# Kernel optimization log

Hardware: AMD Instinct MI355X
Metric: run time of the kernel (lower is better)

## Reference

```python
import jax, jax.numpy as jnp
import numpy as np

N_BRANCH, N_LAYER = 4, 3
B, T, D_IN = 4, 1024, 32
D_MODEL, D_INNER, D_STATE, D_CONV, DT_RANK = 128, 256, 16, 4, 8
EMBED = 64
MAX_NORM = 10.0  # safe_expmap0 tangent-norm clip
EPS = 1e-7


def setup_inputs() -> dict:
    key = jax.random.key(0)
    ks = jax.random.split(key, 12)
    def nrm(k, shp, s=0.02):
        return s * jax.random.normal(k, shp, dtype=jnp.float32)
    A_init = jnp.log(jnp.arange(1, D_STATE + 1, dtype=jnp.float32))
    return {
        "trend": jax.random.normal(ks[0], (B, T, D_IN), jnp.float32),
        "seasonal_coarse": jax.random.normal(ks[1], (B, T, D_IN), jnp.float32),
        "seasonal_fine": jax.random.normal(ks[2], (B, T, D_IN), jnp.float32),
        "residual": jax.random.normal(ks[3], (B, T, D_IN), jnp.float32),
        "W_ip": nrm(ks[4], (N_BRANCH, D_IN, D_MODEL)),
        "b_ip": jnp.zeros((N_BRANCH, D_MODEL), jnp.float32),
        "W_in": nrm(ks[5], (N_BRANCH, N_LAYER, D_MODEL, 2 * D_INNER)),
        "conv_w": nrm(ks[6], (N_BRANCH, N_LAYER, D_INNER, D_CONV), 0.1),
        "conv_b": jnp.zeros((N_BRANCH, N_LAYER, D_INNER), jnp.float32),
        "W_x": nrm(ks[7], (N_BRANCH, N_LAYER, D_INNER, DT_RANK + 2 * D_STATE)),
        "W_dt": nrm(ks[8], (N_BRANCH, N_LAYER, DT_RANK, D_INNER), 0.1),
        "b_dt": jnp.full((N_BRANCH, N_LAYER, D_INNER), -4.6, jnp.float32),  # softplus ~ 0.01
        "A_log": jnp.broadcast_to(A_init, (N_BRANCH, N_LAYER, D_INNER, D_STATE)),
        "D_param": jnp.ones((N_BRANCH, N_LAYER, D_INNER), jnp.float32),
        "W_out": nrm(ks[9], (N_BRANCH, N_LAYER, D_INNER, D_MODEL)),
        "W_op": nrm(ks[10], (N_BRANCH, D_MODEL, EMBED)),
        "b_op": jnp.zeros((N_BRANCH, EMBED), jnp.float32),
        "eff_scale": jnp.asarray(0.1, jnp.float32),
    }


def _mamba_layer(x, Win, cw, cb, Wx, Wdt, bdt, Alog, Dp, Wout):
    # x: [B, T, d_model]
    Tlen = x.shape[1]
    xz = x @ Win                                   # [B,T,2*di]
    xp, z = jnp.split(xz, 2, axis=-1)
    # causal depthwise conv1d, kernel D_CONV
    xpad = jnp.pad(xp, ((0, 0), (D_CONV - 1, 0), (0, 0)))
    xc = sum(xpad[:, k:k + Tlen, :] * cw[:, k] for k in range(D_CONV))
    xc = jax.nn.silu(xc + cb)                      # [B,T,di]
    dbl = xc @ Wx                                  # [B,T,r+2s]
    dt = jax.nn.softplus(dbl[..., :DT_RANK] @ Wdt + bdt)   # [B,T,di]
    Bm = dbl[..., DT_RANK:DT_RANK + D_STATE]       # [B,T,s]
    Cm = dbl[..., DT_RANK + D_STATE:]              # [B,T,s]
    A = -jnp.exp(Alog)                             # [di,s]
    dA = jnp.exp(dt[..., None] * A)                # [B,T,di,s]
    dBx = (dt * xc)[..., None] * Bm[:, :, None, :] # [B,T,di,s]

    def step(h, inp):
        dA_t, dBx_t, C_t = inp
        h = dA_t * h + dBx_t
        return h, jnp.einsum('bds,bs->bd', h, C_t)

    h0 = jnp.zeros((x.shape[0], D_INNER, D_STATE), x.dtype)
    _, ys = jax.lax.scan(step, h0, (jnp.swapaxes(dA, 0, 1),
                                     jnp.swapaxes(dBx, 0, 1),
                                     jnp.swapaxes(Cm, 0, 1)))
    y = jnp.swapaxes(ys, 0, 1) + Dp * xc
    return (y * jax.nn.silu(z)) @ Wout


def _embed(x, Wip, bip, Wins, cws, cbs, Wxs, Wdts, bdts, Alogs, Dps, Wouts, Wop, bop):
    h = x @ Wip + bip
    for l in range(N_LAYER):
        h = _mamba_layer(h, Wins[l], cws[l], cbs[l], Wxs[l], Wdts[l], bdts[l],
                         Alogs[l], Dps[l], Wouts[l])
    return h.mean(axis=1) @ Wop + bop              # [B, EMBED]


def _expmap0(v):
    # safe expmap0 on Lorentz (k=1): clip tangent norm at MAX_NORM
    n = jnp.linalg.norm(v, axis=-1, keepdims=True)
    nc = jnp.clip(n, EPS, MAX_NORM)
    v = v * (nc / jnp.maximum(n, EPS))
    return jnp.concatenate([jnp.cosh(nc), jnp.sinh(nc) / nc * v], axis=-1)


def _projx(x):
    sp = x[..., 1:]
    t = jnp.sqrt(1.0 + jnp.sum(sp * sp, axis=-1, keepdims=True))
    return jnp.concatenate([t, sp], axis=-1)


def _logmap0(x):
    sp = x[..., 1:]
    t = jnp.maximum(x[..., :1], 1.0 + EPS)
    d = jnp.arccosh(t)
    spn = jnp.maximum(jnp.linalg.norm(sp, axis=-1, keepdims=True), EPS)
    return d * sp / spn


def _forward(trend, seasonal_coarse, seasonal_fine, residual,
             W_ip, b_ip, W_in, conv_w, conv_b, W_x, W_dt, b_dt,
             A_log, D_param, W_out, W_op, b_op, eff_scale):
    xs = [trend, seasonal_coarse, seasonal_fine, residual]
    z_t = [
        _embed(xs[b], W_ip[b], b_ip[b], W_in[b], conv_w[b], conv_b[b], W_x[b],
               W_dt[b], b_dt[b], A_log[b], D_param[b], W_out[b], W_op[b], b_op[b])
        for b in range(N_BRANCH)
    ]
    es = jnp.tanh(eff_scale)
    z_h = [_projx(_expmap0(z * es)) for z in z_t]
    us = [_logmap0(zh) for zh in z_h]
    combined_tangent = us[0] + us[1] + us[2] + us[3]
    combined_h = _projx(_expmap0(combined_tangent * es))
    return (*z_t, *z_h, combined_tangent, combined_h)


def reference(trend, seasonal_coarse, seasonal_fine, residual,
              W_ip, b_ip, W_in, conv_w, conv_b, W_x, W_dt, b_dt,
              A_log, D_param, W_out, W_op, b_op, eff_scale):
    return _forward(trend, seasonal_coarse, seasonal_fine, residual,
                    W_ip, b_ip, W_in, conv_w, conv_b, W_x, W_dt, b_dt,
                    A_log, D_param, W_out, W_op, b_op, eff_scale)
```

## Files before the change

kernel.cpp:

```cpp
#include <hip/hip_runtime.h>
#include <math.h>

#define NBR 4
#define NLAY 3
#define Bk 4
#define Tk 1024
#define DIN 32
#define DMODEL 128
#define DINNER 256
#define DSTATE 16
#define DTRANK 8
#define EMBEDk 64
#define BT (Bk*Tk)
#define EPSF 1e-7f
#define MAXNF 10.0f
#define LCH 64
#define NCH (Tk/LCH)
#define UF 8
#define NWB 320

typedef __bf16 bf16x8 __attribute__((ext_vector_type(8)));
typedef float  f32x4  __attribute__((ext_vector_type(4)));
typedef unsigned short u16x8 __attribute__((ext_vector_type(8)));

__device__ __forceinline__ float siluf(float x){ return x / (1.f + __expf(-x)); }
__device__ __forceinline__ float softplusf(float x){ return (x > 20.f) ? x : log1pf(__expf(x)); }
__device__ __forceinline__ unsigned short f2b(float x){
    union { float f; unsigned u; } v; v.f = x;
    unsigned r = v.u + 0x7FFF + ((v.u >> 16) & 1);
    return (unsigned short)(r >> 16);
}
__device__ __forceinline__ float b2f(unsigned short u){
    union { unsigned u; float f; } v; v.u = ((unsigned)u) << 16; return v.f;
}

__device__ __forceinline__ void gll16(const void* g, void* l){
    __builtin_amdgcn_global_load_lds(
        (const __attribute__((address_space(1))) unsigned int*)g,
        (__attribute__((address_space(3))) unsigned int*)l,
        16, 0, 0);
}

__device__ __forceinline__ void dA_pow(float q, float* dA){
    dA[0] = q;             dA[1] = q * q;
    dA[2] = dA[1] * dA[0]; dA[3] = dA[1] * dA[1];
    dA[4] = dA[3] * dA[0]; dA[5] = dA[3] * dA[1];
    dA[6] = dA[3] * dA[2]; dA[7] = dA[3] * dA[3];
    #pragma unroll
    for (int s = 8; s < 16; ++s) dA[s] = dA[s - 8] * dA[7];
}
__device__ __forceinline__ void dA_exp(float dtv, const float* Aa, float* dA){
    #pragma unroll
    for (int s = 0; s < 16; ++s) dA[s] = __expf(dtv * Aa[s]);
}

template<int MODE>
__global__ __launch_bounds__(256) void bgemm_k(
    const unsigned short* __restrict__ Ab, long aBr, int K,
    const unsigned short* __restrict__ Bt, long bBr,
    float* __restrict__ C0, long c0Br,
    float* __restrict__ C1, long c1Br,
    unsigned short* __restrict__ Cb, long cbBr,
    const float* __restrict__ bias, long biasBr)
{
    const int br = blockIdx.z;
    Ab += (long)br * aBr;
    Bt += (long)br * bBr;
    if (MODE == 3) C0 += (long)br * c0Br;
    if (MODE == 0 || MODE == 3) C1 += (long)br * c1Br;
    if (MODE == 0) Cb += (long)br * cbBr;
    if (MODE == 3) bias += (long)br * biasBr;
    const int m0 = blockIdx.x * 64, n0 = blockIdx.y * 64;
    __shared__ __align__(16) unsigned short As[8 * 64 * 8];
    __shared__ __align__(16) unsigned short Bs[8 * 64 * 8];
    const int tid = threadIdx.x;
    const int lane = tid & 63, w = tid >> 6;
    const int wm = w >> 1, wn = w & 1;
    const int quad = lane >> 4, l15 = lane & 15;
    f32x4 acc00 = {0,0,0,0}, acc01 = {0,0,0,0}, acc10 = {0,0,0,0}, acc11 = {0,0,0,0};
    for (int kc = 0; kc < K; kc += 64) {
        #pragma unroll
        for (int it = 0; it < 2; ++it) {
            const int kch = w + it * 4;
            gll16(Ab + (long)(m0 + lane) * K + kc + kch * 8, &As[(kch * 64) * 8]);
            gll16(Bt + (long)(n0 + lane) * K + kc + kch * 8, &Bs[(kch * 64) * 8]);
        }
        __syncthreads();
        #pragma unroll
        for (int k0 = 0; k0 < 64; k0 += 32) {
            const int kch = (k0 >> 3) + quad;
            bf16x8 a0 = *(const bf16x8*)&As[(kch * 64 + wm * 32 +      l15) * 8];
            bf16x8 a1 = *(const bf16x8*)&As[(kch * 64 + wm * 32 + 16 + l15) * 8];
            bf16x8 b0 = *(const bf16x8*)&Bs[(kch * 64 + wn * 32 +      l15) * 8];
            bf16x8 b1 = *(const bf16x8*)&Bs[(kch * 64 + wn * 32 + 16 + l15) * 8];
            acc00 = __builtin_amdgcn_mfma_f32_16x16x32_bf16(a0, b0, acc00, 0, 0, 0);
            acc01 = __builtin_amdgcn_mfma_f32_16x16x32_bf16(a0, b1, acc01, 0, 0, 0);
            acc10 = __builtin_amdgcn_mfma_f32_16x16x32_bf16(a1, b0, acc10, 0, 0, 0);
            acc11 = __builtin_amdgcn_mfma_f32_16x16x32_bf16(a1, b1, acc11, 0, 0, 0);
        }
        __syncthreads();
    }
    #pragma unroll
    for (int e = 0; e < 4; ++e) {
        f32x4 a = (e == 0) ? acc00 : (e == 1) ? acc01 : (e == 2) ? acc10 : acc11;
        const int msub = (e >> 1) * 16, nsub = (e & 1) * 16;
        const int col = n0 + wn * 32 + nsub + l15;
        #pragma unroll
        for (int r = 0; r < 4; ++r) {
            const int row = m0 + wm * 32 + msub + quad * 4 + r;
            const float v = a[r];
            if (MODE == 0) {
                if (n0 < 256) Cb[(long)row * 256 + col] = f2b(v);
                else          C1[(long)row * 256 + (col - 256)] = siluf(v);
            } else {
                if (col < 256)      C0[(long)row * 256 + col] = softplusf(v + bias[col]);
                else if (col < 288) C1[(long)row * 32 + (col - 256)] = v;
            }
        }
    }
}

__global__ __launch_bounds__(256) void prepT_k(
    const float* __restrict__ W, unsigned short* __restrict__ o,
    int Kd, int Nd, long wBr, long oBr)
{
    const int br = blockIdx.z;
    W += (long)br * wBr; o += (long)br * oBr;
    const int n0 = blockIdx.x * 64, k0 = blockIdx.y * 64;
    __shared__ float tile[64][65];
    const int t = threadIdx.x;
    #pragma unroll
    for (int i = 0; i < 16; ++i) {
        int idx = t + i * 256;
        int kl = idx >> 6, nl = idx & 63;
        tile[kl][nl] = W[(long)(k0 + kl) * Nd + n0 + nl];
    }
    __syncthreads();
    #pragma unroll
    for (int i = 0; i < 16; ++i) {
        int idx = t + i * 256;
        int nl = idx >> 6, kl = idx & 63;
        o[(long)(n0 + nl) * Kd + k0 + kl] = f2b(tile[kl][nl]);
    }
}

__global__ __launch_bounds__(256) void sgemmW_k(
    const float* __restrict__ Wout, const float* __restrict__ Win,
    float* __restrict__ Wtmp)
{
    const int z = blockIdx.z, p = z >> 2, br = z & 3;
    const float* A  = Wout + (long)(br * NLAY + p) * DINNER * DMODEL;
    const float* Bw = Win  + (long)(br * NLAY + p + 1) * DMODEL * 512;
    float* C = Wtmp + (long)z * DINNER * 512;
    const int m0 = blockIdx.x * 64, n0 = blockIdx.y * 64;
    __shared__ float As[32][68];
    __shared__ float Bs[32][68];
    const int tid = threadIdx.x;
    const int tx = tid & 15, ty = tid >> 4;
    float acc[4][4] = {};
    for (int kc = 0; kc < DMODEL; kc += 32) {
        #pragma unroll
        for (int it = 0; it < 2; ++it) {
            int id = tid + it * 256;
            int r = id >> 3, c4 = (id & 7) << 2;
            float4 v = *(const float4*)(A + (long)(m0 + r) * DMODEL + kc + c4);
            As[c4+0][r] = v.x; As[c4+1][r] = v.y; As[c4+2][r] = v.z; As[c4+3][r] = v.w;
            int rb = id >> 4, cb = (id & 15) << 2;
            *(float4*)&Bs[rb][cb] = *(const float4*)(Bw + (long)(kc + rb) * 512 + n0 + cb);
        }
        __syncthreads();
        #pragma unroll
        for (int kk = 0; kk < 32; ++kk) {
            float4 a4 = *(const float4*)&As[kk][ty << 2];
            float4 b4 = *(const float4*)&Bs[kk][tx << 2];
            float av[4] = {a4.x, a4.y, a4.z, a4.w};
            float bv[4] = {b4.x, b4.y, b4.z, b4.w};
            #pragma unroll
            for (int i = 0; i < 4; ++i)
                #pragma unroll
                for (int j = 0; j < 4; ++j)
                    acc[i][j] = fmaf(av[i], bv[j], acc[i][j]);
        }
        __syncthreads();
    }
    #pragma unroll
    for (int i = 0; i < 4; ++i) {
        int row = m0 + (ty << 2) + i, col = n0 + (tx << 2);
        float4 v4; v4.x = acc[i][0]; v4.y = acc[i][1]; v4.z = acc[i][2]; v4.w = acc[i][3];
        *(float4*)(C + (long)row * 512 + col) = v4;
    }
}

__global__ __launch_bounds__(256) void prepC_k(
    const float* __restrict__ Wx, const float* __restrict__ Wdt,
    unsigned short* __restrict__ o)
{
    const int n = blockIdx.x, bl = blockIdx.y;
    const int k = threadIdx.x;
    const float* WxP = Wx + (long)bl * DINNER * 40;
    float v;
    if (n < 256) {
        const float* WdtP = Wdt + (long)bl * DTRANK * DINNER;
        float s = 0.f;
        #pragma unroll
        for (int r = 0; r < 8; ++r) s = fmaf(WxP[k * 40 + r], WdtP[r * DINNER + n], s);
        v = s;
    } else if (n < 288) {
        v = WxP[k * 40 + 8 + (n - 256)];
    } else {
        v = 0.f;
    }
    o[(long)bl * NWB * DINNER + (long)n * DINNER + k] = f2b(v);
}

__global__ __launch_bounds__(256) void proj_k(
    const float* __restrict__ A0, const float* __restrict__ A1,
    const float* __restrict__ A2, const float* __restrict__ A3,
    const float* __restrict__ Bw, const float* __restrict__ bias,
    unsigned short* __restrict__ Cb)
{
    const int br = blockIdx.z;
    const float* A = (br == 1) ? A1 : (br == 2) ? A2 : (br == 3) ? A3 : A0;
    Bw   += (long)br * DIN * DMODEL;
    bias += (long)br * DMODEL;
    Cb   += (long)br * BT * DMODEL;
    const int m0 = blockIdx.x * 64, n0 = blockIdx.y * 64;
    __shared__ float As[32][68];
    __shared__ float Bs[32][68];
    const int tid = threadIdx.x;
    const int tx = tid & 15, ty = tid >> 4;
    float acc[4][4] = {};
    {
        #pragma unroll
        for (int it = 0; it < 2; ++it) {
            int id = tid + it * 256;
            int r = id >> 3, c4 = (id & 7) << 2;
            float4 v = *(const float4*)(A + (long)(m0 + r) * DIN + c4);
            As[c4+0][r] = v.x; As[c4+1][r] = v.y; As[c4+2][r] = v.z; As[c4+3][r] = v.w;
            int rb = id >> 4, cb = (id & 15) << 2;
            *(float4*)&Bs[rb][cb] = *(const float4*)(Bw + (long)rb * DMODEL + n0 + cb);
        }
        __syncthreads();
        #pragma unroll
        for (int kk = 0; kk < 32; ++kk) {
            float4 a4 = *(const float4*)&As[kk][ty << 2];
            float4 b4 = *(const float4*)&Bs[kk][tx << 2];
            float av[4] = {a4.x, a4.y, a4.z, a4.w};
            float bv[4] = {b4.x, b4.y, b4.z, b4.w};
            #pragma unroll
            for (int i = 0; i < 4; ++i)
                #pragma unroll
                for (int j = 0; j < 4; ++j)
                    acc[i][j] = fmaf(av[i], bv[j], acc[i][j]);
        }
    }
    const int col = n0 + (tx << 2);
    float bs[4];
    #pragma unroll
    for (int j = 0; j < 4; ++j) bs[j] = bias[col + j];
    #pragma unroll
    for (int i = 0; i < 4; ++i) {
        const int row = m0 + (ty << 2) + i;
        #pragma unroll
        for (int j = 0; j < 4; ++j)
            Cb[(long)row * DMODEL + col + j] = f2b(acc[i][j] + bs[j]);
    }
}

__global__ __launch_bounds__(256) void conv_k(
    const unsigned short* __restrict__ xp, const float* __restrict__ cw,
    const float* __restrict__ cb, unsigned short* __restrict__ xcb, int layer)
{
    const int br = blockIdx.y;
    const long base = (long)br * BT * DINNER;
    const long idx8 = ((long)blockIdx.x * 256 + threadIdx.x) * 8;
    const int d0 = (int)(idx8 & (DINNER - 1));
    const long row = idx8 >> 8;
    const int t = (int)(row & (Tk - 1));
    const float* cwp = cw + ((long)(br * NLAY + layer) * DINNER + d0) * 4;
    const float* cbp = cb + (long)(br * NLAY + layer) * DINNER + d0;
    u16x8 in[4];
    #pragma unroll
    for (int k = 0; k < 4; ++k) {
        const int tt = t + k - 3;
        if (tt >= 0) {
            in[k] = *(const u16x8*)(xp + base + idx8 + (long)(k - 3) * DINNER);
        } else {
            #pragma unroll
            for (int j = 0; j < 8; ++j) in[k][j] = 0;
        }
    }
    u16x8 o;
    #pragma unroll
    for (int j = 0; j < 8; ++j) {
        float acc = cbp[j];
        #pragma unroll
        for (int k = 0; k < 4; ++k)
            acc = fmaf(b2f(in[k][j]), cwp[j * 4 + k], acc);
        o[j] = f2b(siluf(acc));
    }
    *(u16x8*)(xcb + base + idx8) = o;
}

__global__ __launch_bounds__(256) void scan1_k(
    const float* __restrict__ dtb, const unsigned short* __restrict__ xcb,
    const float* __restrict__ bcb, const float* __restrict__ Alog,
    float* __restrict__ recbuf, int layer)
{
    const int c = blockIdx.x, b = blockIdx.y, br = blockIdx.z;
    const int d = threadIdx.x;
    const float* Ap = Alog + ((long)(br * NLAY + layer) * DINNER + d) * DSTATE;
    float Aa[16];
    bool pw = true;
    #pragma unroll
    for (int s = 0; s < 16; ++s) {
        Aa[s] = -__expf(Ap[s]);
        pw = pw && (fabsf(Aa[s] + (float)(s + 1)) < 1e-3f);
    }
    const long rbase = (long)br * BT + (long)b * Tk + (long)c * LCH;
    const float* dtp = dtb + rbase * DINNER + d;
    const unsigned short* xcp = xcb + rbase * DINNER + d;
    __shared__ float bcs[LCH * 32];
    {
        const float4* g = (const float4*)(bcb + rbase * 32);
        float4* l = (float4*)bcs;
        l[d] = g[d]; l[d + 256] = g[d + 256];
    }
    float dtc[UF], xcc[UF];
    #pragma unroll
    for (int u = 0; u < UF; ++u) {
        dtc[u] = dtp[(long)u * DINNER];
        xcc[u] = b2f(xcp[(long)u * DINNER]);
    }
    __syncthreads();
    float h[16];
    #pragma unroll
    for (int s = 0; s < 16; ++s) h[s] = 0.f;
    float sumdt = 0.f;
    for (int base = 0; base < LCH; base += UF) {
        const int nb = (base + UF < LCH) ? base + UF : base;
        float dtn[UF], xcn[UF];
        #pragma unroll
        for (int u = 0; u < UF; ++u) {
            dtn[u] = dtp[(long)(nb + u) * DINNER];
            xcn[u] = b2f(xcp[(long)(nb + u) * DINNER]);
        }
        #pragma unroll
        for (int u = 0; u < UF; ++u) {
            const int t = base + u;
            const float dtv = dtc[u];
            const float dtxc = dtv * xcc[u];
            sumdt += dtv;
            float dA[16];
            if (pw) dA_pow(__expf(-dtv), dA);
            else    dA_exp(dtv, Aa, dA);
            const float* bcT = bcs + t * 32;
            #pragma unroll
            for (int s = 0; s < 16; ++s)
                h[s] = fmaf(dA[s], h[s], dtxc * bcT[s]);
        }
        #pragma unroll
        for (int u = 0; u < UF; ++u) { dtc[u] = dtn[u]; xcc[u] = xcn[u]; }
    }
    float* sb = recbuf + (((long)(br * 4 + b) * (NCH - 1) + c) * 17) * 256 + d;
    #pragma unroll
    for (int s = 0; s < 16; ++s) sb[s * 256] = h[s];
    sb[16 * 256] = sumdt;
}

__global__ __launch_bounds__(256) void scan3_k(
    const float* __restrict__ dtb, const unsigned short* __restrict__ xcb,
    const float* __restrict__ bcb, const float* __restrict__ zb,
    const float* __restrict__ Alog, const float* __restrict__ Dpar,
    const float* __restrict__ recbuf, unsigned short* __restrict__ yzb, int layer)
{
    const int c = blockIdx.x, b = blockIdx.y, br = blockIdx.z;
    const int d = threadIdx.x;
    const float* Ap = Alog + ((long)(br * NLAY + layer) * DINNER + d) * DSTATE;
    float Aa[16];
    bool pw = true;
    #pragma unroll
    for (int s = 0; s < 16; ++s) {
        Aa[s] = -__expf(Ap[s]);
        pw = pw && (fabsf(Aa[s] + (float)(s + 1)) < 1e-3f);
    }
    float h[16];
    #pragma unroll
    for (int s = 0; s < 16; ++s) h[s] = 0.f;
    if (c > 0) {
        const float* recB = recbuf + ((long)(br * 4 + b) * (NCH - 1)) * 17 * 256 + d;
        float rh[16], rs;
        #pragma unroll
        for (int s = 0; s < 16; ++s) rh[s] = recB[s * 256];
        rs = recB[16 * 256];
        for (int cc = 0; cc < c; ++cc) {
            float nh[16], ns = 0.f;
            if (cc + 1 < c) {
                const float* r2 = recB + (long)(cc + 1) * 17 * 256;
                #pragma unroll
                for (int s = 0; s < 16; ++s) nh[s] = r2[s * 256];
                ns = r2[16 * 256];
            } else {
                #pragma unroll
                for (int s = 0; s < 16; ++s) nh[s] = 0.f;
            }
            float P[16];
            if (pw) dA_pow(__expf(-rs), P);
            else    dA_exp(rs, Aa, P);
            #pragma unroll
            for (int s = 0; s < 16; ++s) h[s] = fmaf(h[s], P[s], rh[s]);
            #pragma unroll
            for (int s = 0; s < 16; ++s) rh[s] = nh[s];
            rs = ns;
        }
    }
    const float Dp = Dpar[(br * NLAY + layer) * DINNER + d];
    const long rbase = (long)br * BT + (long)b * Tk + (long)c * LCH;
    const float* dtp = dtb + rbase * DINNER + d;
    const unsigned short* xcp = xcb + rbase * DINNER + d;
    const float* zp  = zb  + rbase * DINNER + d;
    unsigned short* yp = yzb + rbase * DINNER + d;
    __shared__ float bcs[LCH * 32];
    {
        const float4* g = (const float4*)(bcb + rbase * 32);
        float4* l = (float4*)bcs;
        l[d] = g[d]; l[d + 256] = g[d + 256];
    }
    float dtc[UF], xcc[UF], zc[UF];
    #pragma unroll
    for (int u = 0; u < UF; ++u) {
        dtc[u] = dtp[(long)u * DINNER];
        xcc[u] = b2f(xcp[(long)u * DINNER]);
        zc[u]  = zp[(long)u * DINNER];
    }
    __syncthreads();
    for (int base = 0; base < LCH; base += UF) {
        const int nb = (base + UF < LCH) ? base + UF : base;
        float dtn[UF], xcn[UF], zn[UF];
        #pragma unroll
        for (int u = 0; u < UF; ++u) {
            dtn[u] = dtp[(long)(nb + u) * DINNER];
            xcn[u] = b2f(xcp[(long)(nb + u) * DINNER]);
            zn[u]  = zp[(long)(nb + u) * DINNER];
        }
        #pragma unroll
        for (int u = 0; u < UF; ++u) {
            const int t = base + u;
            const float dtv = dtc[u], xcv = xcc[u];
            const float dtxc = dtv * xcv;
            float dA[16];
            if (pw) dA_pow(__expf(-dtv), dA);
            else    dA_exp(dtv, Aa, dA);
            const float* bcT = bcs + t * 32;
            #pragma unroll
            for (int s = 0; s < 16; ++s)
                h[s] = fmaf(dA[s], h[s], dtxc * bcT[s]);
            float y0 = 0.f, y1 = 0.f, y2 = 0.f, y3 = 0.f;
            #pragma unroll
            for (int s = 0; s < 16; s += 4) {
                y0 = fmaf(h[s+0], bcT[16+s+0], y0);
                y1 = fmaf(h[s+1], bcT[16+s+1], y1);
                y2 = fmaf(h[s+2], bcT[16+s+2], y2);
                y3 = fmaf(h[s+3], bcT[16+s+3], y3);
            }
            const float y = (y0 + y1) + (y2 + y3) + Dp * xcv;
            yp[(long)t * DINNER] = f2b(y * zc[u]);
        }
        #pragma unroll
        for (int u = 0; u < UF; ++u) { dtc[u] = dtn[u]; xcc[u] = xcn[u]; zc[u] = zn[u]; }
    }
}

__global__ __launch_bounds__(256) void csum1_k(
    const unsigned short* __restrict__ yz, float* __restrict__ part)
{
    const int ch = blockIdx.x, brb = blockIdx.y;
    const int br = brb >> 2, b = brb & 3;
    const long rbase = (long)br * BT + (long)b * Tk + (long)ch * 128;
    const int tid = threadIdx.x;
    const int cg = tid & 31;
    const int ro = tid >> 5;
    const unsigned short* p = yz + (rbase + ro) * DINNER + cg * 8;
    float acc[8] = {0,0,0,0,0,0,0,0};
    for (int it = 0; it < 16; ++it) {
        u16x8 v = *(const u16x8*)(p + (long)it * 8 * DINNER);
        #pragma unroll
        for (int j = 0; j < 8; ++j) acc[j] += b2f(v[j]);
    }
    __shared__ float sm[8][256];
    #pragma unroll
    for (int j = 0; j < 8; ++j) sm[ro][cg * 8 + j] = acc[j];
    __syncthreads();
    float s = 0.f;
    #pragma unroll
    for (int r = 0; r < 8; ++r) s += sm[r][tid];
    part[((long)brb * 8 + ch) * 256 + tid] = s;
}

__global__ __launch_bounds__(256) void csum2_k(
    const float* __restrict__ part, const float* __restrict__ Wout,
    const float* __restrict__ Wop, const float* __restrict__ bop,
    float* __restrict__ outzt)
{
    const int brb = blockIdx.x;
    const int br = brb >> 2, b = brb & 3;
    const int tid = threadIdx.x;
    __shared__ float v[256];
    __shared__ float u[128];
    float s = 0.f;
    #pragma unroll
    for (int ch = 0; ch < 8; ++ch) s += part[((long)brb * 8 + ch) * 256 + tid];
    v[tid] = s * (1.0f / Tk);
    __syncthreads();
    if (tid < 128) {
        const float* W2 = Wout + (long)(br * NLAY + 2) * DINNER * DMODEL;
        float a = 0.f;
        for (int k = 0; k < 256; ++k) a = fmaf(v[k], W2[k * DMODEL + tid], a);
        u[tid] = a;
    }
    __syncthreads();
    if (tid < EMBEDk) {
        float a = bop[br * EMBEDk + tid];
        for (int k = 0; k < 128; ++k)
            a = fmaf(u[k], Wop[(long)br * DMODEL * EMBEDk + k * EMBEDk + tid], a);
        outzt[br * (Bk * EMBEDk) + b * EMBEDk + tid] = a;
    }
}

__global__ __launch_bounds__(64) void final_k(
    const float* __restrict__ zt, float* __restrict__ out, const float* __restrict__ eff)
{
    const float es = tanhf(eff[0]);
    __shared__ float us[NBR][Bk][EMBEDk];
    const int t = threadIdx.x;
    if (t < 16) {
        const int br = t >> 2, b = t & 3;
        const float* z = zt + br * (Bk * EMBEDk) + b * EMBEDk;
        float n2 = 0.f;
        for (int e = 0; e < EMBEDk; ++e) { float v = z[e] * es; n2 = fmaf(v, v, n2); }
        const float n  = sqrtf(n2);
        const float nc = fminf(fmaxf(n, EPSF), MAXNF);
        const float sc = nc / fmaxf(n, EPSF);
        const float sh = sinhf(nc) / nc;
        const float fac = es * sc * sh;
        float* zh = out + 1024 + br * (Bk * (EMBEDk + 1)) + b * (EMBEDk + 1);
        float sp2 = 0.f;
        for (int e = 0; e < EMBEDk; ++e) {
            float spv = z[e] * fac;
            sp2 = fmaf(spv, spv, sp2);
            zh[1 + e] = spv;
            us[br][b][e] = spv;
        }
        const float t0 = sqrtf(1.f + sp2);
        zh[0] = t0;
        const float dd  = acoshf(fmaxf(t0, 1.f + EPSF));
        const float spn = fmaxf(sqrtf(sp2), EPSF);
        const float rr  = dd / spn;
        for (int e = 0; e < EMBEDk; ++e) us[br][b][e] *= rr;
    }
    __syncthreads();
    if (t < 4) {
        const int b = t;
        float ct[EMBEDk];
        float* cto = out + 2064 + b * EMBEDk;
        for (int e = 0; e < EMBEDk; ++e) {
            float v = us[0][b][e] + us[1][b][e] + us[2][b][e] + us[3][b][e];
            ct[e] = v; cto[e] = v;
        }
        float n2 = 0.f;
        for (int e = 0; e < EMBEDk; ++e) { float v = ct[e] * es; n2 = fmaf(v, v, n2); }
        const float n  = sqrtf(n2);
        const float nc = fminf(fmaxf(n, EPSF), MAXNF);
        const float sc = nc / fmaxf(n, EPSF);
        const float sh = sinhf(nc) / nc;
        const float fac = es * sc * sh;
        float* ch = out + 2320 + b * (EMBEDk + 1);
        float sp2 = 0.f;
        for (int e = 0; e < EMBEDk; ++e) {
            float spv = ct[e] * fac;
            sp2 = fmaf(spv, spv, sp2);
            ch[1 + e] = spv;
        }
        ch[0] = sqrtf(1.f + sp2);
    }
}

extern "C" void kernel_launch(void* const* d_in, const int* in_sizes, int n_in,
                              void* d_out, int out_size, void* d_ws, size_t ws_size,
                              hipStream_t stream)
{
    const float* X0 = (const float*)d_in[0];
    const float* X1 = (const float*)d_in[1];
    const float* X2 = (const float*)d_in[2];
    const float* X3 = (const float*)d_in[3];
    const float* W_ip   = (const float*)d_in[4];
    const float* b_ip   = (const float*)d_in[5];
    const float* W_in   = (const float*)d_in[6];
    const float* conv_w = (const float*)d_in[7];
    const float* conv_b = (const float*)d_in[8];
    const float* W_x    = (const float*)d_in[9];
    const float* W_dt   = (const float*)d_in[10];
    const float* b_dt   = (const float*)d_in[11];
    const float* A_log  = (const float*)d_in[12];
    const float* D_par  = (const float*)d_in[13];
    const float* W_out  = (const float*)d_in[14];
    const float* W_op   = (const float*)d_in[15];
    const float* b_op   = (const float*)d_in[16];
    const float* eff    = (const float*)d_in[17];
    float* out = (float*)d_out;
    float* ws  = (float*)d_ws;

    float* buf_z  = ws;
    float* buf_dt = buf_z  + (long)NBR * BT * DINNER;
    float* buf_bc = buf_dt + (long)NBR * BT * DINNER;
    float* part   = buf_bc + (long)NBR * BT * 32;
    float* recbuf = part   + (long)NBR * BT * DMODEL;
    float* Wtmp   = recbuf + (long)16 * (NCH - 1) * 17 * 256;
    unsigned short* h_bf  = (unsigned short*)(Wtmp + (long)8 * DINNER * 512);
    unsigned short* xp_bf = h_bf  + (long)NBR * BT * DMODEL;
    unsigned short* xc_bf = xp_bf + (long)NBR * BT * DINNER;
    unsigned short* yz_bf = xc_bf + (long)NBR * BT * DINNER;
    unsigned short* Win0T = yz_bf + (long)NBR * BT * DINNER;
    unsigned short* WfT   = Win0T + (long)NBR * 512 * DMODEL;
    unsigned short* WcT   = WfT   + (long)8 * 512 * DINNER;

    prepT_k<<<dim3(8, 2, NBR), 256, 0, stream>>>(
        W_in, Win0T, DMODEL, 512, (long)NLAY * DMODEL * 512, (long)512 * DMODEL);
    sgemmW_k<<<dim3(4, 8, 8), 256, 0, stream>>>(W_out, W_in, Wtmp);
    prepT_k<<<dim3(8, 4, 8), 256, 0, stream>>>(
        Wtmp, WfT, DINNER, 512, (long)DINNER * 512, (long)512 * DINNER);
    prepC_k<<<dim3(NWB, NBR * NLAY), 256, 0, stream>>>(W_x, W_dt, WcT);

    proj_k<<<dim3(BT / 64, DMODEL / 64, NBR), 256, 0, stream>>>(
        X0, X1, X2, X3, W_ip, b_ip, h_bf);

    for (int l = 0; l < NLAY; ++l) {
        if (l == 0) {
            bgemm_k<0><<<dim3(BT / 64, 8, NBR), 256, 0, stream>>>(
                h_bf, (long)BT * DMODEL, DMODEL,
                Win0T, (long)512 * DMODEL,
                nullptr, 0, buf_z, (long)BT * DINNER,
                xp_bf, (long)BT * DINNER, nullptr, 0);
        } else {
            bgemm_k<0><<<dim3(BT / 64, 8, NBR), 256, 0, stream>>>(
                yz_bf, (long)BT * DINNER, DINNER,
                WfT + (long)(l - 1) * 4 * 512 * DINNER, (long)512 * DINNER,
                nullptr, 0, buf_z, (long)BT * DINNER,
                xp_bf, (long)BT * DINNER, nullptr, 0);
        }
        conv_k<<<dim3((BT * DINNER) / (256 * 8), NBR), 256, 0, stream>>>(
            xp_bf, conv_w, conv_b, xc_bf, l);
        bgemm_k<3><<<dim3(BT / 64, NWB / 64, NBR), 256, 0, stream>>>(
            xc_bf, (long)BT * DINNER, DINNER,
            WcT + (long)l * NWB * DINNER, (long)NLAY * NWB * DINNER,
            buf_dt, (long)BT * DINNER, buf_bc, (long)BT * 32,
            nullptr, 0, b_dt + l * DINNER, (long)NLAY * DINNER);
        scan1_k<<<dim3(NCH - 1, Bk, NBR), 256, 0, stream>>>(
            buf_dt, xc_bf, buf_bc, A_log, recbuf, l);
        scan3_k<<<dim3(NCH, Bk, NBR), 256, 0, stream>>>(
            buf_dt, xc_bf, buf_bc, buf_z, A_log, D_par, recbuf, yz_bf, l);
    }

    csum1_k<<<dim3(8, 16), 256, 0, stream>>>(yz_bf, part);
    csum2_k<<<16, 256, 0, stream>>>(part, W_out, W_op, b_op, out);
    final_k<<<1, 64, 0, stream>>>(out, out, eff);
}
```

Measured before the change: 425.1 us.

## Fuse conv, x-projection GEMM and chunked scan into one flag-chained kernel

Conv1d, the dt/B/C projection GEMM, softplus and the selective scan now run in one per-chunk kernel. It keeps xc, dt and B/C in shared memory and passes chunk carry state between blocks through global flags instead of separate scan passes. The input projection is folded into the first layer's in-projection weights, so the first layer skips an intermediate GEMM and its activations. The weight pre-transposes are merged into the weight-fusion GEMM, and the final reduction kernels are combined into one. This cuts launches and intermediate global traffic, but adds serialized inter-block waits on flags and heavy shared-memory use per block.

```diff
diff --git a/kernel.cpp b/kernel.cpp
--- a/kernel.cpp
+++ b/kernel.cpp
@@ -18,10 +18,12 @@
 #define NCH (Tk/LCH)
 #define UF 8
 #define NWB 320
+#define DTS 257
 
 typedef __bf16 bf16x8 __attribute__((ext_vector_type(8)));
 typedef float  f32x4  __attribute__((ext_vector_type(4)));
 typedef unsigned short u16x8 __attribute__((ext_vector_type(8)));
+typedef unsigned short u16x4 __attribute__((ext_vector_type(4)));
 
 __device__ __forceinline__ float siluf(float x){ return x / (1.f + __expf(-x)); }
 __device__ __forceinline__ float softplusf(float x){ return (x > 20.f) ? x : log1pf(__expf(x)); }
@@ -54,22 +56,17 @@
     for (int s = 0; s < 16; ++s) dA[s] = __expf(dtv * Aa[s]);
 }
 
-template<int MODE>
-__global__ __launch_bounds__(256) void bgemm_k(
+__global__ __launch_bounds__(256) void xzgemm_k(
     const unsigned short* __restrict__ Ab, long aBr, int K,
     const unsigned short* __restrict__ Bt, long bBr,
-    float* __restrict__ C0, long c0Br,
     float* __restrict__ C1, long c1Br,
-    unsigned short* __restrict__ Cb, long cbBr,
-    const float* __restrict__ bias, long biasBr)
+    unsigned short* __restrict__ Cb, long cbBr)
 {
     const int br = blockIdx.z;
     Ab += (long)br * aBr;
     Bt += (long)br * bBr;
-    if (MODE == 3) C0 += (long)br * c0Br;
-    if (MODE == 0 || MODE == 3) C1 += (long)br * c1Br;
-    if (MODE == 0) Cb += (long)br * cbBr;
-    if (MODE == 3) bias += (long)br * biasBr;
+    C1 += (long)br * c1Br;
+    Cb += (long)br * cbBr;
     const int m0 = blockIdx.x * 64, n0 = blockIdx.y * 64;
     __shared__ __align__(16) unsigned short As[8 * 64 * 8];
     __shared__ __align__(16) unsigned short Bs[8 * 64 * 8];
@@ -109,85 +106,106 @@
         for (int r = 0; r < 4; ++r) {
             const int row = m0 + wm * 32 + msub + quad * 4 + r;
             const float v = a[r];
-            if (MODE == 0) {
-                if (n0 < 256) Cb[(long)row * 256 + col] = f2b(v);
-                else          C1[(long)row * 256 + (col - 256)] = siluf(v);
-            } else {
-                if (col < 256)      C0[(long)row * 256 + col] = softplusf(v + bias[col]);
-                else if (col < 288) C1[(long)row * 32 + (col - 256)] = v;
-            }
-        }
-    }
-}
-
-__global__ __launch_bounds__(256) void prepT_k(
-    const float* __restrict__ W, unsigned short* __restrict__ o,
-    int Kd, int Nd, long wBr, long oBr)
+            if (n0 < 256) Cb[(long)row * 256 + col] = f2b(v);
+            else          C1[(long)row * 256 + (col - 256)] = siluf(v);
+        }
+    }
+}
+
+__global__ __launch_bounds__(256) void sgemmWT_k(
+    const float* __restrict__ Wout, const float* __restrict__ Win,
+    const float* __restrict__ Wip, const float* __restrict__ bip,
+    unsigned short* __restrict__ WfT, float* __restrict__ Weq)
 {
-    const int br = blockIdx.z;
-    W += (long)br * wBr; o += (long)br * oBr;
-    const int n0 = blockIdx.x * 64, k0 = blockIdx.y * 64;
-    __shared__ float tile[64][65];
-    const int t = threadIdx.x;
-    #pragma unroll
-    for (int i = 0; i < 16; ++i) {
-        int idx = t + i * 256;
-        int kl = idx >> 6, nl = idx & 63;
-        tile[kl][nl] = W[(long)(k0 + kl) * Nd + n0 + nl];
-    }
-    __syncthreads();
-    #pragma unroll
-    for (int i = 0; i < 16; ++i) {
-        int idx = t + i * 256;
-        int nl = idx >> 6, kl = idx & 63;
-        o[(long)(n0 + nl) * Kd + k0 + kl] = f2b(tile[kl][nl]);
-    }
-}
-
-__global__ __launch_bounds__(256) void sgemmW_k(
-    const float* __restrict__ Wout, const float* __restrict__ Win,
-    float* __restrict__ Wtmp)
-{
-    const int z = blockIdx.z, p = z >> 2, br = z & 3;
-    const float* A  = Wout + (long)(br * NLAY + p) * DINNER * DMODEL;
-    const float* Bw = Win  + (long)(br * NLAY + p + 1) * DMODEL * 512;
-    float* C = Wtmp + (long)z * DINNER * 512;
-    const int m0 = blockIdx.x * 64, n0 = blockIdx.y * 64;
-    __shared__ float As[32][68];
-    __shared__ float Bs[32][68];
+    const int z = blockIdx.z;
     const int tid = threadIdx.x;
     const int tx = tid & 15, ty = tid >> 4;
+    __shared__ float As_[32][68];
+    __shared__ float Bs_[32][68];
     float acc[4][4] = {};
-    for (int kc = 0; kc < DMODEL; kc += 32) {
-        #pragma unroll
-        for (int it = 0; it < 2; ++it) {
-            int id = tid + it * 256;
-            int r = id >> 3, c4 = (id & 7) << 2;
-            float4 v = *(const float4*)(A + (long)(m0 + r) * DMODEL + kc + c4);
-            As[c4+0][r] = v.x; As[c4+1][r] = v.y; As[c4+2][r] = v.z; As[c4+3][r] = v.w;
-            int rb = id >> 4, cb = (id & 15) << 2;
-            *(float4*)&Bs[rb][cb] = *(const float4*)(Bw + (long)(kc + rb) * 512 + n0 + cb);
-        }
-        __syncthreads();
-        #pragma unroll
-        for (int kk = 0; kk < 32; ++kk) {
-            float4 a4 = *(const float4*)&As[kk][ty << 2];
-            float4 b4 = *(const float4*)&Bs[kk][tx << 2];
-            float av[4] = {a4.x, a4.y, a4.z, a4.w};
-            float bv[4] = {b4.x, b4.y, b4.z, b4.w};
-            #pragma unroll
-            for (int i = 0; i < 4; ++i)
-                #pragma unroll
-                for (int j = 0; j < 4; ++j)
-                    acc[i][j] = fmaf(av[i], bv[j], acc[i][j]);
-        }
-        __syncthreads();
-    }
-    #pragma unroll
-    for (int i = 0; i < 4; ++i) {
-        int row = m0 + (ty << 2) + i, col = n0 + (tx << 2);
-        float4 v4; v4.x = acc[i][0]; v4.y = acc[i][1]; v4.z = acc[i][2]; v4.w = acc[i][3];
-        *(float4*)(C + (long)row * 512 + col) = v4;
+    if (z < 8) {
+        const int p = z >> 2, br = z & 3;
+        const float* A  = Wout + (long)(br * NLAY + p) * DINNER * DMODEL;
+        const float* Bw = Win  + (long)(br * NLAY + p + 1) * DMODEL * 512;
+        const int m0 = blockIdx.x * 64, n0 = blockIdx.y * 64;
+        for (int kc = 0; kc < DMODEL; kc += 32) {
+            #pragma unroll
+            for (int it = 0; it < 2; ++it) {
+                int id = tid + it * 256;
+                int r = id >> 3, c4 = (id & 7) << 2;
+                float4 v = *(const float4*)(A + (long)(m0 + r) * DMODEL + kc + c4);
+                As_[c4+0][r] = v.x; As_[c4+1][r] = v.y; As_[c4+2][r] = v.z; As_[c4+3][r] = v.w;
+                int rb = id >> 4, cb = (id & 15) << 2;
+                *(float4*)&Bs_[rb][cb] = *(const float4*)(Bw + (long)(kc + rb) * 512 + n0 + cb);
+            }
+            __syncthreads();
+            #pragma unroll
+            for (int kk = 0; kk < 32; ++kk) {
+                float4 a4 = *(const float4*)&As_[kk][ty << 2];
+                float4 b4 = *(const float4*)&Bs_[kk][tx << 2];
+                float av[4] = {a4.x, a4.y, a4.z, a4.w};
+                float bv[4] = {b4.x, b4.y, b4.z, b4.w};
+                #pragma unroll
+                for (int i = 0; i < 4; ++i)
+                    #pragma unroll
+                    for (int j = 0; j < 4; ++j)
+                        acc[i][j] = fmaf(av[i], bv[j], acc[i][j]);
+            }
+            __syncthreads();
+        }
+        unsigned short* o = WfT + (long)z * 512 * 256;
+        const int row0 = m0 + (ty << 2), col = n0 + (tx << 2);
+        #pragma unroll
+        for (int j = 0; j < 4; ++j) {
+            u16x4 v;
+            #pragma unroll
+            for (int i = 0; i < 4; ++i) v[i] = f2b(acc[i][j]);
+            *(u16x4*)(o + (long)(col + j) * 256 + row0) = v;
+        }
+    } else {
+        const int br = blockIdx.x;
+        const float* A  = Wip + (long)br * DIN * DMODEL;
+        const float* bp = bip + (long)br * DMODEL;
+        const float* Bw = Win + (long)br * NLAY * DMODEL * 512;
+        const int n0 = blockIdx.y * 64;
+        for (int kc = 0; kc < DMODEL; kc += 32) {
+            #pragma unroll
+            for (int it = 0; it < 2; ++it) {
+                int id = tid + it * 256;
+                int r = id >> 3, c4 = (id & 7) << 2;
+                float4 v;
+                if (r < 32)       v = *(const float4*)(A + (long)r * DMODEL + kc + c4);
+                else if (r == 32) v = *(const float4*)(bp + kc + c4);
+                else              { v.x = 0.f; v.y = 0.f; v.z = 0.f; v.w = 0.f; }
+                As_[c4+0][r] = v.x; As_[c4+1][r] = v.y; As_[c4+2][r] = v.z; As_[c4+3][r] = v.w;
+                int rb = id >> 4, cb = (id & 15) << 2;
+                *(float4*)&Bs_[rb][cb] = *(const float4*)(Bw + (long)(kc + rb) * 512 + n0 + cb);
+            }
+            __syncthreads();
+            #pragma unroll
+            for (int kk = 0; kk < 32; ++kk) {
+                float4 a4 = *(const float4*)&As_[kk][ty << 2];
+                float4 b4 = *(const float4*)&Bs_[kk][tx << 2];
+                float av[4] = {a4.x, a4.y, a4.z, a4.w};
+                float bv[4] = {b4.x, b4.y, b4.z, b4.w};
+                #pragma unroll
+                for (int i = 0; i < 4; ++i)
+                    #pragma unroll
+                    for (int j = 0; j < 4; ++j)
+                        acc[i][j] = fmaf(av[i], bv[j], acc[i][j]);
+            }
+            __syncthreads();
+        }
+        float* C = Weq + (long)br * 33 * 512;
+        const int col = n0 + (tx << 2);
+        #pragma unroll
+        for (int i = 0; i < 4; ++i) {
+            const int row = (ty << 2) + i;
+            if (row < 33) {
+                float4 v4; v4.x = acc[i][0]; v4.y = acc[i][1]; v4.z = acc[i][2]; v4.w = acc[i][3];
+                *(float4*)(C + (long)row * 512 + col) = v4;
+            }
+        }
     }
 }
 
@@ -213,20 +231,20 @@
     o[(long)bl * NWB * DINNER + (long)n * DINNER + k] = f2b(v);
 }
 
-__global__ __launch_bounds__(256) void proj_k(
+__global__ __launch_bounds__(256) void xgemm0_k(
     const float* __restrict__ A0, const float* __restrict__ A1,
     const float* __restrict__ A2, const float* __restrict__ A3,
-    const float* __restrict__ Bw, const float* __restrict__ bias,
-    unsigned short* __restrict__ Cb)
+    const float* __restrict__ Weq,
+    float* __restrict__ zb, unsigned short* __restrict__ xpb)
 {
     const int br = blockIdx.z;
     const float* A = (br == 1) ? A1 : (br == 2) ? A2 : (br == 3) ? A3 : A0;
-    Bw   += (long)br * DIN * DMODEL;
-    bias += (long)br * DMODEL;
-    Cb   += (long)br * BT * DMODEL;
+    const float* W = Weq + (long)br * 33 * 512;
+    float* C1 = zb + (long)br * BT * DINNER;
+    unsigned short* Cb = xpb + (long)br * BT * DINNER;
     const int m0 = blockIdx.x * 64, n0 = blockIdx.y * 64;
-    __shared__ float As[32][68];
-    __shared__ float Bs[32][68];
+    __shared__ float As_[32][68];
+    __shared__ float Bs_[32][68];
     const int tid = threadIdx.x;
     const int tx = tid & 15, ty = tid >> 4;
     float acc[4][4] = {};
@@ -236,15 +254,15 @@
             int id = tid + it * 256;
             int r = id >> 3, c4 = (id & 7) << 2;
             float4 v = *(const float4*)(A + (long)(m0 + r) * DIN + c4);
-            As[c4+0][r] = v.x; As[c4+1][r] = v.y; As[c4+2][r] = v.z; As[c4+3][r] = v.w;
+            As_[c4+0][r] = v.x; As_[c4+1][r] = v.y; As_[c4+2][r] = v.z; As_[c4+3][r] = v.w;
             int rb = id >> 4, cb = (id & 15) << 2;
-            *(float4*)&Bs[rb][cb] = *(const float4*)(Bw + (long)rb * DMODEL + n0 + cb);
+            *(float4*)&Bs_[rb][cb] = *(const float4*)(W + (long)rb * 512 + n0 + cb);
         }
         __syncthreads();
         #pragma unroll
         for (int kk = 0; kk < 32; ++kk) {
-            float4 a4 = *(const float4*)&As[kk][ty << 2];
-            float4 b4 = *(const float4*)&Bs[kk][tx << 2];
+            float4 a4 = *(const float4*)&As_[kk][ty << 2];
+            float4 b4 = *(const float4*)&Bs_[kk][tx << 2];
             float av[4] = {a4.x, a4.y, a4.z, a4.w};
             float bv[4] = {b4.x, b4.y, b4.z, b4.w};
             #pragma unroll
@@ -255,140 +273,189 @@
         }
     }
     const int col = n0 + (tx << 2);
-    float bs[4];
-    #pragma unroll
-    for (int j = 0; j < 4; ++j) bs[j] = bias[col + j];
+    float be[4];
+    #pragma unroll
+    for (int j = 0; j < 4; ++j) be[j] = W[32 * 512 + col + j];
     #pragma unroll
     for (int i = 0; i < 4; ++i) {
         const int row = m0 + (ty << 2) + i;
         #pragma unroll
-        for (int j = 0; j < 4; ++j)
-            Cb[(long)row * DMODEL + col + j] = f2b(acc[i][j] + bs[j]);
-    }
-}
-
-__global__ __launch_bounds__(256) void conv_k(
-    const unsigned short* __restrict__ xp, const float* __restrict__ cw,
-    const float* __restrict__ cb, unsigned short* __restrict__ xcb, int layer)
-{
-    const int br = blockIdx.y;
-    const long base = (long)br * BT * DINNER;
-    const long idx8 = ((long)blockIdx.x * 256 + threadIdx.x) * 8;
-    const int d0 = (int)(idx8 & (DINNER - 1));
-    const long row = idx8 >> 8;
-    const int t = (int)(row & (Tk - 1));
-    const float* cwp = cw + ((long)(br * NLAY + layer) * DINNER + d0) * 4;
-    const float* cbp = cb + (long)(br * NLAY + layer) * DINNER + d0;
-    u16x8 in[4];
-    #pragma unroll
-    for (int k = 0; k < 4; ++k) {
-        const int tt = t + k - 3;
-        if (tt >= 0) {
-            in[k] = *(const u16x8*)(xp + base + idx8 + (long)(k - 3) * DINNER);
-        } else {
-            #pragma unroll
-            for (int j = 0; j < 8; ++j) in[k][j] = 0;
-        }
-    }
-    u16x8 o;
-    #pragma unroll
-    for (int j = 0; j < 8; ++j) {
-        float acc = cbp[j];
-        #pragma unroll
-        for (int k = 0; k < 4; ++k)
-            acc = fmaf(b2f(in[k][j]), cwp[j * 4 + k], acc);
-        o[j] = f2b(siluf(acc));
-    }
-    *(u16x8*)(xcb + base + idx8) = o;
-}
-
-__global__ __launch_bounds__(256) void scan1_k(
-    const float* __restrict__ dtb, const unsigned short* __restrict__ xcb,
-    const float* __restrict__ bcb, const float* __restrict__ Alog,
-    float* __restrict__ recbuf, int layer)
+        for (int j = 0; j < 4; ++j) {
+            const float v = acc[i][j] + be[j];
+            if (n0 < 256) Cb[(long)row * 256 + col + j] = f2b(v);
+            else          C1[(long)row * 256 + (col - 256 + j)] = siluf(v);
+        }
+    }
+}
+
+__global__ __launch_bounds__(256) void dtscan_k(
+    const unsigned short* __restrict__ xp, const float* __restrict__ zb,
+    const unsigned short* __restrict__ WcT,
+    const float* __restrict__ cw, const float* __restrict__ cbias,
+    const float* __restrict__ bdtA, const float* __restrict__ Alog,
+    const float* __restrict__ Dpar, float* __restrict__ recbuf,
+    int* __restrict__ flags, unsigned short* __restrict__ yzb, int layer)
 {
     const int c = blockIdx.x, b = blockIdx.y, br = blockIdx.z;
-    const int d = threadIdx.x;
-    const float* Ap = Alog + ((long)(br * NLAY + layer) * DINNER + d) * DSTATE;
-    float Aa[16];
-    bool pw = true;
+    const int tid = threadIdx.x;
+    const int lane = tid & 63, w = tid >> 6;
+    const int bl = br * NLAY + layer;
+
+    __shared__ __align__(16) unsigned short As[32 * 64 * 8];
+    __shared__ __align__(16) unsigned short Bs[8 * 320 * 8];
+    __shared__ float dts[64 * DTS];
+    __shared__ float bcs[64 * 32];
+
+    const long rbase = (long)br * BT + (long)b * Tk + (long)c * LCH;
+
+    {
+        const int g = tid & 31, r0 = tid >> 5;
+        const int d0 = g * 8;
+        float wv[8][4], bv[8];
+        #pragma unroll
+        for (int j = 0; j < 8; ++j) {
+            const float4 w4 = *(const float4*)(cw + ((long)bl * DINNER + d0 + j) * 4);
+            wv[j][0] = w4.x; wv[j][1] = w4.y; wv[j][2] = w4.z; wv[j][3] = w4.w;
+            bv[j] = cbias[bl * DINNER + d0 + j];
+        }
+        const unsigned short* xpb = xp + ((long)br * BT + (long)b * Tk) * DINNER + d0;
+        #pragma unroll
+        for (int i = 0; i < 8; ++i) {
+            const int r = r0 + i * 8;
+            const int tg = c * LCH + r;
+            u16x8 in[4];
+            #pragma unroll
+            for (int k = 0; k < 4; ++k) {
+                const int tt = tg + k - 3;
+                if (tt >= 0) {
+                    in[k] = *(const u16x8*)(xpb + (long)tt * DINNER);
+                } else {
+                    #pragma unroll
+                    for (int j = 0; j < 8; ++j) in[k][j] = 0;
+                }
+            }
+            u16x8 o;
+            #pragma unroll
+            for (int j = 0; j < 8; ++j) {
+                float a = bv[j];
+                #pragma unroll
+                for (int k = 0; k < 4; ++k) a = fmaf(b2f(in[k][j]), wv[j][k], a);
+                o[j] = f2b(siluf(a));
+            }
+            *(u16x8*)&As[((g * 64) + (r ^ (g & 7))) * 8] = o;
+        }
+    }
+    __syncthreads();
+
+    const int wm = w >> 1, wn = w & 1;
+    const int quad = lane >> 4, l15 = lane & 15;
+    f32x4 acc[5][4];
+    #pragma unroll
+    for (int nt = 0; nt < 5; ++nt)
+        #pragma unroll
+        for (int e = 0; e < 4; ++e) { f32x4 zz = {0,0,0,0}; acc[nt][e] = zz; }
+    {
+        const unsigned short* Bt = WcT + (long)bl * NWB * DINNER;
+        for (int kc = 0; kc < 4; ++kc) {
+            #pragma unroll
+            for (int i = 0; i < 10; ++i) {
+                const int unit = w * 10 + i;
+                const int kch = unit / 5, nblk = unit % 5;
+                gll16(Bt + (long)(nblk * 64 + lane) * DINNER + kc * 64 + kch * 8,
+                      &Bs[(kch * 320 + nblk * 64) * 8]);
+            }
+            __syncthreads();
+            #pragma unroll
+            for (int k0 = 0; k0 < 2; ++k0) {
+                const int kchL = k0 * 4 + quad;
+                const int kchG = kc * 8 + kchL;
+                const int xr = kchG & 7;
+                bf16x8 a0 = *(const bf16x8*)&As[(kchG * 64 + ((wm * 32 + l15) ^ xr)) * 8];
+                bf16x8 a1 = *(const bf16x8*)&As[(kchG * 64 + ((wm * 32 + 16 + l15) ^ xr)) * 8];
+                #pragma unroll
+                for (int nt = 0; nt < 5; ++nt) {
+                    bf16x8 b0 = *(const bf16x8*)&Bs[(kchL * 320 + nt * 64 + wn * 32 + l15) * 8];
+                    bf16x8 b1 = *(const bf16x8*)&Bs[(kchL * 320 + nt * 64 + wn * 32 + 16 + l15) * 8];
+                    acc[nt][0] = __builtin_amdgcn_mfma_f32_16x16x32_bf16(a0, b0, acc[nt][0], 0, 0, 0);
+                    acc[nt][1] = __builtin_amdgcn_mfma_f32_16x16x32_bf16(a0, b1, acc[nt][1], 0, 0, 0);
+                    acc[nt][2] = __builtin_amdgcn_mfma_f32_16x16x32_bf16(a1, b0, acc[nt][2], 0, 0, 0);
+                    acc[nt][3] = __builtin_amdgcn_mfma_f32_16x16x32_bf16(a1, b1, acc[nt][3], 0, 0, 0);
+                }
+            }
+            __syncthreads();
+        }
+    }
+    {
+        const float* bdt = bdtA + (long)bl * DINNER;
+        #pragma unroll
+        for (int nt = 0; nt < 5; ++nt) {
+            #pragma unroll
+            for (int e = 0; e < 4; ++e) {
+                const f32x4 a = acc[nt][e];
+                const int msub = (e >> 1) * 16, nsub = (e & 1) * 16;
+                const int col = nt * 64 + wn * 32 + nsub + l15;
+                #pragma unroll
+                for (int r = 0; r < 4; ++r) {
+                    const int row = wm * 32 + msub + quad * 4 + r;
+                    if (col < 256)      dts[row * DTS + col] = softplusf(a[r] + bdt[col]);
+                    else if (col < 288) bcs[row * 32 + (col - 256)] = a[r];
+                }
+            }
+        }
+    }
+    __syncthreads();
+
+    const int d = tid;
+    const float* Ap = Alog + ((long)bl * DINNER + d) * DSTATE;
+    float Aa[16]; bool pw = true;
     #pragma unroll
     for (int s = 0; s < 16; ++s) {
         Aa[s] = -__expf(Ap[s]);
         pw = pw && (fabsf(Aa[s] + (float)(s + 1)) < 1e-3f);
     }
-    const long rbase = (long)br * BT + (long)b * Tk + (long)c * LCH;
-    const float* dtp = dtb + rbase * DINNER + d;
-    const unsigned short* xcp = xcb + rbase * DINNER + d;
-    __shared__ float bcs[LCH * 32];
-    {
-        const float4* g = (const float4*)(bcb + rbase * 32);
-        float4* l = (float4*)bcs;
-        l[d] = g[d]; l[d + 256] = g[d + 256];
-    }
-    float dtc[UF], xcc[UF];
-    #pragma unroll
-    for (int u = 0; u < UF; ++u) {
-        dtc[u] = dtp[(long)u * DINNER];
-        xcc[u] = b2f(xcp[(long)u * DINNER]);
-    }
-    __syncthreads();
-    float h[16];
-    #pragma unroll
-    for (int s = 0; s < 16; ++s) h[s] = 0.f;
-    float sumdt = 0.f;
-    for (int base = 0; base < LCH; base += UF) {
-        const int nb = (base + UF < LCH) ? base + UF : base;
-        float dtn[UF], xcn[UF];
-        #pragma unroll
-        for (int u = 0; u < UF; ++u) {
-            dtn[u] = dtp[(long)(nb + u) * DINNER];
-            xcn[u] = b2f(xcp[(long)(nb + u) * DINNER]);
-        }
-        #pragma unroll
-        for (int u = 0; u < UF; ++u) {
-            const int t = base + u;
-            const float dtv = dtc[u];
-            const float dtxc = dtv * xcc[u];
+    const int kchX = d >> 3, jX = d & 7, kxor = kchX & 7;
+    const int gidx = (br * 4 + b) * 16;
+    const long recstride = 17 * 256;
+
+    if (c < NCH - 1) {
+        float h[16];
+        #pragma unroll
+        for (int s = 0; s < 16; ++s) h[s] = 0.f;
+        float sumdt = 0.f;
+        #pragma unroll 4
+        for (int t = 0; t < LCH; ++t) {
+            const float dtv = dts[t * DTS + d];
+            const float xcv = b2f(As[(kchX * 64 + (t ^ kxor)) * 8 + jX]);
+            const float dtxc = dtv * xcv;
             sumdt += dtv;
             float dA[16];
-            if (pw) dA_pow(__expf(-dtv), dA);
-            else    dA_exp(dtv, Aa, dA);
+            if (pw) dA_pow(__expf(-dtv), dA); else dA_exp(dtv, Aa, dA);
             const float* bcT = bcs + t * 32;
             #pragma unroll
-            for (int s = 0; s < 16; ++s)
-                h[s] = fmaf(dA[s], h[s], dtxc * bcT[s]);
-        }
-        #pragma unroll
-        for (int u = 0; u < UF; ++u) { dtc[u] = dtn[u]; xcc[u] = xcn[u]; }
-    }
-    float* sb = recbuf + (((long)(br * 4 + b) * (NCH - 1) + c) * 17) * 256 + d;
-    #pragma unroll
-    for (int s = 0; s < 16; ++s) sb[s * 256] = h[s];
-    sb[16 * 256] = sumdt;
-}
-
-__global__ __launch_bounds__(256) void scan3_k(
-    const float* __restrict__ dtb, const unsigned short* __restrict__ xcb,
-    const float* __restrict__ bcb, const float* __restrict__ zb,
-    const float* __restrict__ Alog, const float* __restrict__ Dpar,
-    const float* __restrict__ recbuf, unsigned short* __restrict__ yzb, int layer)
-{
-    const int c = blockIdx.x, b = blockIdx.y, br = blockIdx.z;
-    const int d = threadIdx.x;
-    const float* Ap = Alog + ((long)(br * NLAY + layer) * DINNER + d) * DSTATE;
-    float Aa[16];
-    bool pw = true;
-    #pragma unroll
-    for (int s = 0; s < 16; ++s) {
-        Aa[s] = -__expf(Ap[s]);
-        pw = pw && (fabsf(Aa[s] + (float)(s + 1)) < 1e-3f);
-    }
-    float h[16];
-    #pragma unroll
-    for (int s = 0; s < 16; ++s) h[s] = 0.f;
+            for (int s = 0; s < 16; ++s) h[s] = fmaf(dA[s], h[s], dtxc * bcT[s]);
+        }
+        float* sb = recbuf + (long)(gidx + c) * recstride + d;
+        #pragma unroll
+        for (int s = 0; s < 16; ++s) sb[s * 256] = h[s];
+        sb[16 * 256] = sumdt;
+        __threadfence();
+        __syncthreads();
+        if (tid == 0)
+            __hip_atomic_store(&flags[gidx + c], 1, __ATOMIC_RELEASE, __HIP_MEMORY_SCOPE_AGENT);
+    }
+
+    float hc[16];
+    #pragma unroll
+    for (int s = 0; s < 16; ++s) hc[s] = 0.f;
     if (c > 0) {
-        const float* recB = recbuf + ((long)(br * 4 + b) * (NCH - 1)) * 17 * 256 + d;
+        if (tid == 0) {
+            for (int cc = 0; cc < c; ++cc)
+                while (__hip_atomic_load(&flags[gidx + cc], __ATOMIC_ACQUIRE, __HIP_MEMORY_SCOPE_AGENT) == 0)
+                    __builtin_amdgcn_s_sleep(2);
+        }
+        __syncthreads();
+        __threadfence();
+        const float* recB = recbuf + (long)gidx * recstride + d;
         float rh[16], rs;
         #pragma unroll
         for (int s = 0; s < 16; ++s) rh[s] = recB[s * 256];
@@ -396,7 +463,7 @@
         for (int cc = 0; cc < c; ++cc) {
             float nh[16], ns = 0.f;
             if (cc + 1 < c) {
-                const float* r2 = recB + (long)(cc + 1) * 17 * 256;
+                const float* r2 = recB + (long)(cc + 1) * recstride;
                 #pragma unroll
                 for (int s = 0; s < 16; ++s) nh[s] = r2[s * 256];
                 ns = r2[16 * 256];
@@ -405,69 +472,55 @@
                 for (int s = 0; s < 16; ++s) nh[s] = 0.f;
             }
             float P[16];
-            if (pw) dA_pow(__expf(-rs), P);
-            else    dA_exp(rs, Aa, P);
-            #pragma unroll
-            for (int s = 0; s < 16; ++s) h[s] = fmaf(h[s], P[s], rh[s]);
+            if (pw) dA_pow(__expf(-rs), P); else dA_exp(rs, Aa, P);
+            #pragma unroll
+            for (int s = 0; s < 16; ++s) hc[s] = fmaf(hc[s], P[s], rh[s]);
             #pragma unroll
             for (int s = 0; s < 16; ++s) rh[s] = nh[s];
             rs = ns;
         }
     }
-    const float Dp = Dpar[(br * NLAY + layer) * DINNER + d];
-    const long rbase = (long)br * BT + (long)b * Tk + (long)c * LCH;
-    const float* dtp = dtb + rbase * DINNER + d;
-    const unsigned short* xcp = xcb + rbase * DINNER + d;
-    const float* zp  = zb  + rbase * DINNER + d;
-    unsigned short* yp = yzb + rbase * DINNER + d;
-    __shared__ float bcs[LCH * 32];
+
     {
-        const float4* g = (const float4*)(bcb + rbase * 32);
-        float4* l = (float4*)bcs;
-        l[d] = g[d]; l[d + 256] = g[d + 256];
-    }
-    float dtc[UF], xcc[UF], zc[UF];
-    #pragma unroll
-    for (int u = 0; u < UF; ++u) {
-        dtc[u] = dtp[(long)u * DINNER];
-        xcc[u] = b2f(xcp[(long)u * DINNER]);
-        zc[u]  = zp[(long)u * DINNER];
-    }
-    __syncthreads();
-    for (int base = 0; base < LCH; base += UF) {
-        const int nb = (base + UF < LCH) ? base + UF : base;
-        float dtn[UF], xcn[UF], zn[UF];
-        #pragma unroll
-        for (int u = 0; u < UF; ++u) {
-            dtn[u] = dtp[(long)(nb + u) * DINNER];
-            xcn[u] = b2f(xcp[(long)(nb + u) * DINNER]);
-            zn[u]  = zp[(long)(nb + u) * DINNER];
-        }
-        #pragma unroll
-        for (int u = 0; u < UF; ++u) {
-            const int t = base + u;
-            const float dtv = dtc[u], xcv = xcc[u];
-            const float dtxc = dtv * xcv;
-            float dA[16];
-            if (pw) dA_pow(__expf(-dtv), dA);
-            else    dA_exp(dtv, Aa, dA);
-            const float* bcT = bcs + t * 32;
-            #pragma unroll
-            for (int s = 0; s < 16; ++s)
-                h[s] = fmaf(dA[s], h[s], dtxc * bcT[s]);
-            float y0 = 0.f, y1 = 0.f, y2 = 0.f, y3 = 0.f;
-            #pragma unroll
-            for (int s = 0; s < 16; s += 4) {
-                y0 = fmaf(h[s+0], bcT[16+s+0], y0);
-                y1 = fmaf(h[s+1], bcT[16+s+1], y1);
-                y2 = fmaf(h[s+2], bcT[16+s+2], y2);
-                y3 = fmaf(h[s+3], bcT[16+s+3], y3);
-            }
-            const float y = (y0 + y1) + (y2 + y3) + Dp * xcv;
-            yp[(long)t * DINNER] = f2b(y * zc[u]);
-        }
-        #pragma unroll
-        for (int u = 0; u < UF; ++u) { dtc[u] = dtn[u]; xcc[u] = xcn[u]; zc[u] = zn[u]; }
+        const float Dp = Dpar[bl * DINNER + d];
+        const float* zp = zb + rbase * DINNER + d;
+        unsigned short* yp = yzb + rbase * DINNER + d;
+        float h[16];
+        #pragma unroll
+        for (int s = 0; s < 16; ++s) h[s] = hc[s];
+        float zc[UF];
+        #pragma unroll
+        for (int u = 0; u < UF; ++u) zc[u] = zp[(long)u * DINNER];
+        for (int base = 0; base < LCH; base += UF) {
+            const int nb = (base + UF < LCH) ? base + UF : base;
+            float zn[UF];
+            #pragma unroll
+            for (int u = 0; u < UF; ++u) zn[u] = zp[(long)(nb + u) * DINNER];
+            #pragma unroll
+            for (int u = 0; u < UF; ++u) {
+                const int t = base + u;
+                const float dtv = dts[t * DTS + d];
+                const float xcv = b2f(As[(kchX * 64 + (t ^ kxor)) * 8 + jX]);
+                const float dtxc = dtv * xcv;
+                float dA[16];
+                if (pw) dA_pow(__expf(-dtv), dA); else dA_exp(dtv, Aa, dA);
+                const float* bcT = bcs + t * 32;
+                #pragma unroll
+                for (int s = 0; s < 16; ++s) h[s] = fmaf(dA[s], h[s], dtxc * bcT[s]);
+                float y0 = 0.f, y1 = 0.f, y2 = 0.f, y3 = 0.f;
+                #pragma unroll
+                for (int s = 0; s < 16; s += 4) {
+                    y0 = fmaf(h[s+0], bcT[16+s+0], y0);
+                    y1 = fmaf(h[s+1], bcT[16+s+1], y1);
+                    y2 = fmaf(h[s+2], bcT[16+s+2], y2);
+                    y3 = fmaf(h[s+3], bcT[16+s+3], y3);
+                }
+                const float y = (y0 + y1) + (y2 + y3) + Dp * xcv;
+                yp[(long)t * DINNER] = f2b(y * zc[u]);
+            }
+            #pragma unroll
+            for (int u = 0; u < UF; ++u) zc[u] = zn[u];
+        }
     }
 }
 
@@ -497,45 +550,51 @@
     part[((long)brb * 8 + ch) * 256 + tid] = s;
 }
 
-__global__ __launch_bounds__(256) void csum2_k(
+__global__ __launch_bounds__(256) void csum2f_k(
     const float* __restrict__ part, const float* __restrict__ Wout,
     const float* __restrict__ Wop, const float* __restrict__ bop,
-    float* __restrict__ outzt)
+    const float* __restrict__ eff, float* __restrict__ out)
 {
-    const int brb = blockIdx.x;
-    const int br = brb >> 2, b = brb & 3;
     const int tid = threadIdx.x;
-    __shared__ float v[256];
-    __shared__ float u[128];
-    float s = 0.f;
-    #pragma unroll
-    for (int ch = 0; ch < 8; ++ch) s += part[((long)brb * 8 + ch) * 256 + tid];
-    v[tid] = s * (1.0f / Tk);
+    __shared__ float vm[16][256];
+    __shared__ float um[16][128];
+    __shared__ float zs[16][64];
+    __shared__ float us[NBR][Bk][EMBEDk];
+    #pragma unroll
+    for (int brb = 0; brb < 16; ++brb) {
+        float s = 0.f;
+        #pragma unroll
+        for (int chh = 0; chh < 8; ++chh) s += part[((long)brb * 8 + chh) * 256 + tid];
+        vm[brb][tid] = s * (1.0f / Tk);
+    }
     __syncthreads();
-    if (tid < 128) {
+    #pragma unroll
+    for (int i = 0; i < 8; ++i) {
+        const int idx = tid + i * 256;
+        const int brb = idx >> 7, colu = idx & 127;
+        const int br = brb >> 2;
         const float* W2 = Wout + (long)(br * NLAY + 2) * DINNER * DMODEL;
         float a = 0.f;
-        for (int k = 0; k < 256; ++k) a = fmaf(v[k], W2[k * DMODEL + tid], a);
-        u[tid] = a;
+        for (int k = 0; k < 256; ++k) a = fmaf(vm[brb][k], W2[k * DMODEL + colu], a);
+        um[brb][colu] = a;
     }
     __syncthreads();
-    if (tid < EMBEDk) {
-        float a = bop[br * EMBEDk + tid];
-        for (int k = 0; k < 128; ++k)
-            a = fmaf(u[k], Wop[(long)br * DMODEL * EMBEDk + k * EMBEDk + tid], a);
-        outzt[br * (Bk * EMBEDk) + b * EMBEDk + tid] = a;
-    }
-}
-
-__global__ __launch_bounds__(64) void final_k(
-    const float* __restrict__ zt, float* __restrict__ out, const float* __restrict__ eff)
-{
+    #pragma unroll
+    for (int i = 0; i < 4; ++i) {
+        const int idx = tid + i * 256;
+        const int brb = idx >> 6, e = idx & 63;
+        const int br = brb >> 2;
+        float a = bop[br * EMBEDk + e];
+        for (int k = 0; k < DMODEL; ++k)
+            a = fmaf(um[brb][k], Wop[(long)br * DMODEL * EMBEDk + k * EMBEDk + e], a);
+        zs[brb][e] = a;
+        out[brb * EMBEDk + e] = a;
+    }
+    __syncthreads();
     const float es = tanhf(eff[0]);
-    __shared__ float us[NBR][Bk][EMBEDk];
-    const int t = threadIdx.x;
-    if (t < 16) {
-        const int br = t >> 2, b = t & 3;
-        const float* z = zt + br * (Bk * EMBEDk) + b * EMBEDk;
+    if (tid < 16) {
+        const int br = tid >> 2, b = tid & 3;
+        const float* z = zs[br * 4 + b];
         float n2 = 0.f;
         for (int e = 0; e < EMBEDk; ++e) { float v = z[e] * es; n2 = fmaf(v, v, n2); }
         const float n  = sqrtf(n2);
@@ -559,8 +618,8 @@
         for (int e = 0; e < EMBEDk; ++e) us[br][b][e] *= rr;
     }
     __syncthreads();
-    if (t < 4) {
-        const int b = t;
+    if (tid < 4) {
+        const int b = tid;
         float ct[EMBEDk];
         float* cto = out + 2064 + b * EMBEDk;
         for (int e = 0; e < EMBEDk; ++e) {
@@ -574,14 +633,14 @@
         const float sc = nc / fmaxf(n, EPSF);
         const float sh = sinhf(nc) / nc;
         const float fac = es * sc * sh;
-        float* ch = out + 2320 + b * (EMBEDk + 1);
+        float* chh = out + 2320 + b * (EMBEDk + 1);
         float sp2 = 0.f;
         for (int e = 0; e < EMBEDk; ++e) {
             float spv = ct[e] * fac;
             sp2 = fmaf(spv, spv, sp2);
-            ch[1 + e] = spv;
-        }
-        ch[0] = sqrtf(1.f + sp2);
+            chh[1 + e] = spv;
+        }
+        chh[0] = sqrtf(1.f + sp2);
     }
 }
 
@@ -611,57 +670,36 @@
     float* ws  = (float*)d_ws;
 
     float* buf_z  = ws;
-    float* buf_dt = buf_z  + (long)NBR * BT * DINNER;
-    float* buf_bc = buf_dt + (long)NBR * BT * DINNER;
-    float* part   = buf_bc + (long)NBR * BT * 32;
-    float* recbuf = part   + (long)NBR * BT * DMODEL;
-    float* Wtmp   = recbuf + (long)16 * (NCH - 1) * 17 * 256;
-    unsigned short* h_bf  = (unsigned short*)(Wtmp + (long)8 * DINNER * 512);
-    unsigned short* xp_bf = h_bf  + (long)NBR * BT * DMODEL;
-    unsigned short* xc_bf = xp_bf + (long)NBR * BT * DINNER;
-    unsigned short* yz_bf = xc_bf + (long)NBR * BT * DINNER;
-    unsigned short* Win0T = yz_bf + (long)NBR * BT * DINNER;
-    unsigned short* WfT   = Win0T + (long)NBR * 512 * DMODEL;
+    float* part   = buf_z  + (long)NBR * BT * DINNER;
+    float* recbuf = part   + 32768;
+    float* Weq    = recbuf + (long)256 * 17 * 256;
+    int*   flags  = (int*)(Weq + 67584);
+    unsigned short* xp_bf = (unsigned short*)(flags + 768);
+    unsigned short* yz_bf = xp_bf + (long)NBR * BT * DINNER;
+    unsigned short* WfT   = yz_bf + (long)NBR * BT * DINNER;
     unsigned short* WcT   = WfT   + (long)8 * 512 * DINNER;
 
-    prepT_k<<<dim3(8, 2, NBR), 256, 0, stream>>>(
-        W_in, Win0T, DMODEL, 512, (long)NLAY * DMODEL * 512, (long)512 * DMODEL);
-    sgemmW_k<<<dim3(4, 8, 8), 256, 0, stream>>>(W_out, W_in, Wtmp);
-    prepT_k<<<dim3(8, 4, 8), 256, 0, stream>>>(
-        Wtmp, WfT, DINNER, 512, (long)DINNER * 512, (long)512 * DINNER);
+    hipMemsetAsync(flags, 0, NLAY * 256 * sizeof(int), stream);
+
     prepC_k<<<dim3(NWB, NBR * NLAY), 256, 0, stream>>>(W_x, W_dt, WcT);
-
-    proj_k<<<dim3(BT / 64, DMODEL / 64, NBR), 256, 0, stream>>>(
-        X0, X1, X2, X3, W_ip, b_ip, h_bf);
+    sgemmWT_k<<<dim3(4, 8, 9), 256, 0, stream>>>(W_out, W_in, W_ip, b_ip, WfT, Weq);
+
+    xgemm0_k<<<dim3(BT / 64, 8, NBR), 256, 0, stream>>>(
+        X0, X1, X2, X3, Weq, buf_z, xp_bf);
 
     for (int l = 0; l < NLAY; ++l) {
-        if (l == 0) {
-            bgemm_k<0><<<dim3(BT / 64, 8, NBR), 256, 0, stream>>>(
-                h_bf, (long)BT * DMODEL, DMODEL,
-                Win0T, (long)512 * DMODEL,
-                nullptr, 0, buf_z, (long)BT * DINNER,
-                xp_bf, (long)BT * DINNER, nullptr, 0);
-        } else {
-            bgemm_k<0><<<dim3(BT / 64, 8, NBR), 256, 0, stream>>>(
+        if (l > 0) {
+            xzgemm_k<<<dim3(BT / 64, 8, NBR), 256, 0, stream>>>(
                 yz_bf, (long)BT * DINNER, DINNER,
                 WfT + (long)(l - 1) * 4 * 512 * DINNER, (long)512 * DINNER,
-                nullptr, 0, buf_z, (long)BT * DINNER,
-                xp_bf, (long)BT * DINNER, nullptr, 0);
-        }
-        conv_k<<<dim3((BT * DINNER) / (256 * 8), NBR), 256, 0, stream>>>(
-            xp_bf, conv_w, conv_b, xc_bf, l);
-        bgemm_k<3><<<dim3(BT / 64, NWB / 64, NBR), 256, 0, stream>>>(
-            xc_bf, (long)BT * DINNER, DINNER,
-            WcT + (long)l * NWB * DINNER, (long)NLAY * NWB * DINNER,
-            buf_dt, (long)BT * DINNER, buf_bc, (long)BT * 32,
-            nullptr, 0, b_dt + l * DINNER, (long)NLAY * DINNER);
-        scan1_k<<<dim3(NCH - 1, Bk, NBR), 256, 0, stream>>>(
-            buf_dt, xc_bf, buf_bc, A_log, recbuf, l);
-        scan3_k<<<dim3(NCH, Bk, NBR), 256, 0, stream>>>(
-            buf_dt, xc_bf, buf_bc, buf_z, A_log, D_par, recbuf, yz_bf, l);
+                buf_z, (long)BT * DINNER,
+                xp_bf, (long)BT * DINNER);
+        }
+        dtscan_k<<<dim3(NCH, Bk, NBR), 256, 0, stream>>>(
+            xp_bf, buf_z, WcT, conv_w, conv_b, b_dt, A_log, D_par,
+            recbuf, flags + l * 256, yz_bf, l);
     }
 
     csum1_k<<<dim3(8, 16), 256, 0, stream>>>(yz_bf, part);
-    csum2_k<<<16, 256, 0, stream>>>(part, W_out, W_op, b_op, out);
-    final_k<<<1, 64, 0, stream>>>(out, out, eff);
-}
+    csum2f_k<<<1, 256, 0, stream>>>(part, W_out, W_op, b_op, eff, out);
+}
```

After: 683.5 us. +60.8%, slower.
